# Performance work log

Hardware: AMD Instinct MI355X
Metric: run time of the kernel (lower is better)

## Reference

```python
import jax, jax.numpy as jnp
import numpy as np
import math

E, DK, R = 8, 32, 16        # n_experts, d_k, lora rank
SCALING = 16.0 / 16.0        # lora_alpha / r


def setup_inputs() -> dict:
    key = jax.random.key(0)
    ks = jax.random.split(key, 7)
    Bt, S, Din, Dout = 4, 2048, 4096, 4096
    x = jax.random.normal(ks[0], (Bt, S, Din), jnp.float32)
    W = jax.random.normal(ks[1], (Dout, Din), jnp.float32) * 0.02   # base linear weight
    b = jnp.zeros((Dout,), jnp.float32)
    Wq = jax.random.normal(ks[2], (E * DK, Din), jnp.float32) * 0.02  # query_layer
    Wk = jax.random.normal(ks[3], (E * DK, Din), jnp.float32) * 0.02  # key_layer
    A = jax.random.normal(ks[4], (E, R, Din), jnp.float32) * 0.02     # lora_As stacked
    Bm = jax.random.normal(ks[5], (E, Dout, R), jnp.float32) * 0.02   # lora_Bs stacked (nonzero for testing)
    return {"x": x, "W": W, "b": b, "Wq": Wq, "Wk": Wk, "A": A, "Bm": Bm}


def reference(x, W, b, Wq, Wk, A, Bm):
    Bt, S, Din = x.shape
    # base linear: y = x @ W.T + b
    result = jnp.einsum('bsi,oi->bso', x, W) + b
    # per-expert attention routing scores
    q = jnp.einsum('bsi,ni->bsn', x, Wq).reshape(Bt, S, E, DK)
    k = jnp.einsum('bsi,ni->bsn', x, Wk).reshape(Bt, S, E, DK)
    scores = jnp.einsum('bsed,bsed->bse', q, k) / math.sqrt(DK)
    w = jax.nn.softmax(scores, axis=-1)                      # [b,s,E]
    # per-expert low-rank projection: [b,s,E,r]
    h = jnp.einsum('bsi,eri->bser', x, A)
    # fused weighted combine through lora_B: avoids [b,s,E,out] intermediate
    combined = jnp.einsum('bse,bser,eor->bso', w, h, Bm) * SCALING
    return result + combined
```

## Files before the change

### kernel.cpp

```cpp
#include <hip/hip_runtime.h>
#include <hip/hip_bf16.h>
#include <cstdint>
#include <cstddef>


#define T_TOK   8192
#define DIN     4096
#define DOUT    4096
#define KEXT    4224
#define NQKA    640
#define SCALING 1.0f

typedef __attribute__((ext_vector_type(8))) short bf16x8;
typedef __attribute__((ext_vector_type(4))) float f32x4;

__device__ __forceinline__ unsigned short f2bf(float f) {
    __hip_bfloat16 h = __float2bfloat16(f);
    return *reinterpret_cast<unsigned short*>(&h);
}

__device__ __forceinline__ void load_lds16(const void* g, void* l) {
    __builtin_amdgcn_global_load_lds((__attribute__((address_space(1))) void*)g,
                                     (__attribute__((address_space(3))) void*)l,
                                     16, 0, 0);
}

__global__ __launch_bounds__(256) void conv_x(const float4* __restrict__ x,
                                              unsigned short* __restrict__ Aext) {
    int t = blockIdx.x * 256 + threadIdx.x;
    int row = t >> 10, c4 = t & 1023;
    float4 v = x[(size_t)row * 1024 + c4];
    ushort4 o;
    o.x = f2bf(v.x); o.y = f2bf(v.y); o.z = f2bf(v.z); o.w = f2bf(v.w);
    *(ushort4*)&Aext[(size_t)row * KEXT + c4 * 4] = o;
}

__global__ __launch_bounds__(256) void conv_w(const float4* __restrict__ W,
                                              unsigned short* __restrict__ Wext) {
    int t = blockIdx.x * 256 + threadIdx.x;
    int row = t >> 10, c4 = t & 1023;
    float4 v = W[(size_t)row * 1024 + c4];
    ushort4 o;
    o.x = f2bf(v.x); o.y = f2bf(v.y); o.z = f2bf(v.z); o.w = f2bf(v.w);
    *(ushort4*)&Wext[(size_t)row * KEXT + c4 * 4] = o;
}

__global__ __launch_bounds__(256) void fill_bm(const float* __restrict__ Bm,
                                               unsigned short* __restrict__ Wext) {
    int t = blockIdx.x * 256 + threadIdx.x;
    int o = t >> 7, j = t & 127;
    int e = j >> 4, r = j & 15;
    float v = Bm[(size_t)e * (DOUT * 16) + (size_t)o * 16 + r] * SCALING;
    Wext[(size_t)o * KEXT + DIN + j] = f2bf(v);
}

__global__ __launch_bounds__(256) void conv_wqka(const float4* __restrict__ Wq,
                                                 const float4* __restrict__ Wk,
                                                 const float4* __restrict__ Alora,
                                                 unsigned short* __restrict__ Wqka) {
    int t = blockIdx.x * 256 + threadIdx.x;
    int row = t >> 10, c4 = t & 1023;
    float4 v;
    if (row < 256)       v = Wq[(size_t)row * 1024 + c4];
    else if (row < 512)  v = Wk[(size_t)(row - 256) * 1024 + c4];
    else                 v = Alora[(size_t)(row - 512) * 1024 + c4];
    ushort4 o;
    o.x = f2bf(v.x); o.y = f2bf(v.y); o.z = f2bf(v.z); o.w = f2bf(v.w);
    *(ushort4*)&Wqka[(size_t)row * 4096 + c4 * 4] = o;
}

__global__ __launch_bounds__(64) void routing(const float* __restrict__ P,
                                              unsigned short* __restrict__ Aext) {
    int token = blockIdx.x;
    const float* p = P + (size_t)token * NQKA;
    int l = threadIdx.x;
    int e = l >> 3, s = l & 7;
    float pp = 0.f;
#pragma unroll
    for (int j = 0; j < 4; j++) {
        int d = e * 32 + s * 4 + j;
        pp += p[d] * p[256 + d];
    }
    pp += __shfl_xor(pp, 4);
    pp += __shfl_xor(pp, 2);
    pp += __shfl_xor(pp, 1);
    float score = pp * 0.17677669529663687f;
    float mx = score;
    mx = fmaxf(mx, __shfl_xor(mx, 8));
    mx = fmaxf(mx, __shfl_xor(mx, 16));
    mx = fmaxf(mx, __shfl_xor(mx, 32));
    float ex = expf(score - mx);
    float sm = ex;
    sm += __shfl_xor(sm, 8);
    sm += __shfl_xor(sm, 16);
    sm += __shfl_xor(sm, 32);
    float w = ex / sm;
    __shared__ float sw[8];
    if (s == 0) sw[e] = w;
    __syncthreads();
    unsigned short* g = Aext + (size_t)token * KEXT + DIN;
#pragma unroll
    for (int i = 0; i < 2; i++) {
        int j = l + i * 64;
        float val = sw[j >> 4] * p[512 + j] * SCALING;
        g[j] = f2bf(val);
    }
}

__global__ __launch_bounds__(256, 2)
void gemm_bt(const unsigned short* __restrict__ A,
             const unsigned short* __restrict__ B,
             float* __restrict__ C,
             const float* __restrict__ bias,
             int lda, int ldb, int N, int K) {
    __shared__ unsigned short ldsA[128 * 32];
    __shared__ unsigned short ldsB[128 * 32];
    const int t = threadIdx.x;
    const int m0 = blockIdx.y * 128;
    const int n0 = blockIdx.x * 128;
    const int wave = t >> 6, lane = t & 63;
    const int wm = (wave >> 1) * 64, wn = (wave & 1) * 64;
    const int fr = lane & 15, quad = lane >> 4;

    f32x4 acc[4][4];
#pragma unroll
    for (int i = 0; i < 4; i++)
#pragma unroll
        for (int j = 0; j < 4; j++) acc[i][j] = (f32x4){0.f, 0.f, 0.f, 0.f};

    const unsigned short* aptr = A + (size_t)(m0 + (t >> 2)) * lda + (t & 3) * 8;
    const unsigned short* bptr = B + (size_t)(n0 + (t >> 2)) * ldb + (t & 3) * 8;
    char* ldsAb = (char*)ldsA + t * 16;
    char* ldsBb = (char*)ldsB + t * 16;

    for (int k0 = 0; k0 < K; k0 += 32) {
        load_lds16(aptr, ldsAb);
        load_lds16(aptr + 64 * (size_t)lda, ldsAb + 4096);
        load_lds16(bptr, ldsBb);
        load_lds16(bptr + 64 * (size_t)ldb, ldsBb + 4096);
        aptr += 32; bptr += 32;
        __syncthreads();

        bf16x8 af[4], bfr[4];
#pragma unroll
        for (int i = 0; i < 4; i++)
            af[i] = *(const bf16x8*)(ldsA + (wm + i * 16 + fr) * 32 + quad * 8);
#pragma unroll
        for (int j = 0; j < 4; j++)
            bfr[j] = *(const bf16x8*)(ldsB + (wn + j * 16 + fr) * 32 + quad * 8);
#pragma unroll
        for (int i = 0; i < 4; i++)
#pragma unroll
            for (int j = 0; j < 4; j++)
                acc[i][j] = __builtin_amdgcn_mfma_f32_16x16x32_bf16(af[i], bfr[j], acc[i][j], 0, 0, 0);
        __syncthreads();
    }

#pragma unroll
    for (int j = 0; j < 4; j++) {
        int col = n0 + wn + j * 16 + fr;
        float bv = bias ? bias[col] : 0.f;
#pragma unroll
        for (int i = 0; i < 4; i++) {
            int row0 = m0 + wm + i * 16 + quad * 4;
#pragma unroll
            for (int r = 0; r < 4; r++)
                C[(size_t)(row0 + r) * N + col] = acc[i][j][r] + bv;
        }
    }
}

extern "C" void kernel_launch(void* const* d_in, const int* in_sizes, int n_in,
                              void* d_out, int out_size, void* d_ws, size_t ws_size,
                              hipStream_t stream) {
    const float* x  = (const float*)d_in[0];
    const float* W  = (const float*)d_in[1];
    const float* b  = (const float*)d_in[2];
    const float* Wq = (const float*)d_in[3];
    const float* Wk = (const float*)d_in[4];
    const float* Al = (const float*)d_in[5];
    const float* Bm = (const float*)d_in[6];
    float* out = (float*)d_out;

    char* ws = (char*)d_ws;
    unsigned short* Aext = (unsigned short*)ws;
    unsigned short* Wext = (unsigned short*)(ws + 69206016);
    unsigned short* Wqka = (unsigned short*)(ws + 69206016 + 34603008);
    float*          P    = (float*)(ws + 69206016 + 34603008 + 5242880);

    conv_x   <<<T_TOK * 1024 / 256, 256, 0, stream>>>((const float4*)x, Aext);
    conv_w   <<<DOUT * 1024 / 256, 256, 0, stream>>>((const float4*)W, Wext);
    fill_bm  <<<DOUT * 128 / 256, 256, 0, stream>>>(Bm, Wext);
    conv_wqka<<<NQKA * 1024 / 256, 256, 0, stream>>>((const float4*)Wq, (const float4*)Wk,
                                                     (const float4*)Al, Wqka);

    {
        dim3 grid(NQKA / 128, T_TOK / 128);
        gemm_bt<<<grid, 256, 0, stream>>>(Aext, Wqka, P, nullptr, KEXT, 4096, NQKA, 4096);
    }

    routing<<<T_TOK, 64, 0, stream>>>(P, Aext);

    {
        dim3 grid(DOUT / 128, T_TOK / 128);
        gemm_bt<<<grid, 256, 0, stream>>>(Aext, Wext, out, b, KEXT, KEXT, DOUT, KEXT);
    }
}
```

Before: 723.4 us.

## Replace main GEMM with 256x256-tile, 4-stage pipelined, XCD-swizzled kernel

Adds a new GEMM kernel for the large output projection. It uses 256x256 tiles with 8 waves, a 4-deep LDS ring filled by direct global-to-LDS loads, and XOR-swizzled LDS addressing to reduce bank conflicts. It also remaps blocks round-robin across XCDs and raises MFMA priority with setprio. The goal is to hide memory latency and raise data reuse compared with the unpipelined 128x128 kernel. The cost is more complex waitcnt and barrier logic and more LDS per block, which could limit occupancy or break on edge cases.

Result: faster. 640.5 us (-11.5%).

```diff
diff --git a/kernel.cpp b/kernel.cpp
--- a/kernel.cpp
+++ b/kernel.cpp
@@ -170,6 +170,122 @@
     }
 }
 
+__global__ __launch_bounds__(512, 2)
+void gemm256_8p(const unsigned short* __restrict__ A,
+                const unsigned short* __restrict__ B,
+                float* __restrict__ C,
+                const float* __restrict__ bias,
+                int lda, int ldb, int N, int K, int grid_n) {
+    __shared__ unsigned short lds[65536];
+    const int t = threadIdx.x;
+
+    const int nwg = gridDim.x;
+    const int q8 = nwg >> 3;
+    const int wg = (blockIdx.x & 7) * q8 + (blockIdx.x >> 3);
+    const int m0 = (wg / grid_n) * 256;
+    const int n0 = (wg % grid_n) * 256;
+
+    const int lane = t & 63;
+    const int fr = lane & 15, quad = lane >> 4;
+    const int wr = t >> 8;
+    const int wc = (t >> 6) & 3;
+    const int slot16 = ((quad ^ ((fr >> 1) & 3)) << 4);
+
+    char* ldsA = (char*)lds;
+    char* ldsB = (char*)lds + 65536;
+
+    const int srow = t >> 2;
+    const int sE = ((t & 3) ^ ((t >> 3) & 3)) * 8;
+    const unsigned short* aP = A + (size_t)(m0 + srow) * lda + sE;
+    const unsigned short* bP = B + (size_t)(n0 + srow) * ldb + sE;
+    const size_t a128 = 128 * (size_t)lda, b128 = 128 * (size_t)ldb;
+    char* dA = ldsA + t * 16;
+    char* dB = ldsB + t * 16;
+
+#define STAGE_A(cc) { const unsigned short* g_ = aP + (size_t)(cc) * 32;          \
+        char* d_ = dA + ((cc) & 3) * 16384;                                       \
+        load_lds16(g_, d_); load_lds16(g_ + a128, d_ + 8192); }
+#define STAGE_B(cc) { const unsigned short* g_ = bP + (size_t)(cc) * 32;          \
+        char* d_ = dB + ((cc) & 3) * 16384;                                       \
+        load_lds16(g_, d_); load_lds16(g_ + b128, d_ + 8192); }
+
+    f32x4 acc[8][4];
+#pragma unroll
+    for (int i = 0; i < 8; i++)
+#pragma unroll
+        for (int j = 0; j < 4; j++) acc[i][j] = (f32x4){0.f, 0.f, 0.f, 0.f};
+
+    STAGE_A(0); STAGE_B(0);
+    STAGE_A(1); STAGE_B(1);
+    STAGE_A(2); STAGE_B(2);
+    asm volatile("s_waitcnt vmcnt(8)" ::: "memory");
+    __builtin_amdgcn_s_barrier();
+
+    const int NC = K >> 5;
+    const char* rA = ldsA + wr * 8192 + fr * 64 + slot16;
+    const char* rB = ldsB + wc * 4096 + fr * 64 + slot16;
+
+    for (int c = 0; c < NC; ++c) {
+        const char* cA = rA + (c & 3) * 16384;
+        const char* cB = rB + (c & 3) * 16384;
+        bf16x8 am[4], bn[4];
+
+#pragma unroll
+        for (int i = 0; i < 4; ++i) am[i] = *(const bf16x8*)(cA + i * 1024);
+#pragma unroll
+        for (int i = 0; i < 4; ++i) bn[i] = *(const bf16x8*)(cB + i * 1024);
+        if (c + 3 < NC) STAGE_A(c + 3);
+        __builtin_amdgcn_sched_barrier(0);
+        __builtin_amdgcn_s_barrier();
+        asm volatile("s_waitcnt lgkmcnt(0)" ::: "memory");
+        __builtin_amdgcn_sched_barrier(0);
+        __builtin_amdgcn_s_setprio(1);
+#pragma unroll
+        for (int mf = 0; mf < 4; ++mf)
+#pragma unroll
+            for (int nf = 0; nf < 4; ++nf)
+                acc[mf][nf] = __builtin_amdgcn_mfma_f32_16x16x32_bf16(am[mf], bn[nf], acc[mf][nf], 0, 0, 0);
+        __builtin_amdgcn_s_setprio(0);
+        __builtin_amdgcn_sched_barrier(0);
+        __builtin_amdgcn_s_barrier();
+
+#pragma unroll
+        for (int i = 0; i < 4; ++i) am[i] = *(const bf16x8*)(cA + (4 + i) * 1024);
+        if (c + 3 < NC) STAGE_B(c + 3);
+        __builtin_amdgcn_sched_barrier(0);
+        __builtin_amdgcn_s_barrier();
+        asm volatile("s_waitcnt lgkmcnt(0)" ::: "memory");
+        __builtin_amdgcn_sched_barrier(0);
+        __builtin_amdgcn_s_setprio(1);
+#pragma unroll
+        for (int mf = 0; mf < 4; ++mf)
+#pragma unroll
+            for (int nf = 0; nf < 4; ++nf)
+                acc[4 + mf][nf] = __builtin_amdgcn_mfma_f32_16x16x32_bf16(am[mf], bn[nf], acc[4 + mf][nf], 0, 0, 0);
+        __builtin_amdgcn_s_setprio(0);
+        if (c < NC - 3)       { asm volatile("s_waitcnt vmcnt(8)" ::: "memory"); }
+        else if (c == NC - 3) { asm volatile("s_waitcnt vmcnt(4)" ::: "memory"); }
+        else if (c == NC - 2) { asm volatile("s_waitcnt vmcnt(0)" ::: "memory"); }
+        __builtin_amdgcn_sched_barrier(0);
+        __builtin_amdgcn_s_barrier();
+    }
+
+#pragma unroll
+    for (int nf = 0; nf < 4; ++nf) {
+        int col = n0 + wc * 64 + nf * 16 + fr;
+        float bv = bias ? bias[col] : 0.f;
+#pragma unroll
+        for (int mf = 0; mf < 8; ++mf) {
+            int row0 = m0 + wr * 128 + mf * 16 + quad * 4;
+#pragma unroll
+            for (int r = 0; r < 4; ++r)
+                C[(size_t)(row0 + r) * N + col] = acc[mf][nf][r] + bv;
+        }
+    }
+#undef STAGE_A
+#undef STAGE_B
+}
+
 extern "C" void kernel_launch(void* const* d_in, const int* in_sizes, int n_in,
                               void* d_out, int out_size, void* d_ws, size_t ws_size,
                               hipStream_t stream) {
@@ -202,7 +318,8 @@
     routing<<<T_TOK, 64, 0, stream>>>(P, Aext);
 
     {
-        dim3 grid(DOUT / 128, T_TOK / 128);
-        gemm_bt<<<grid, 256, 0, stream>>>(Aext, Wext, out, b, KEXT, KEXT, DOUT, KEXT);
-    }
-}
+        int grid_n = DOUT / 256;
+        int nwg = (T_TOK / 256) * grid_n;
+        gemm256_8p<<<nwg, 512, 0, stream>>>(Aext, Wext, out, b, KEXT, KEXT, DOUT, KEXT, grid_n);
+    }
+}
```
